# Optimization experiments

Hardware: AMD Instinct MI355X
Metric: run time of the kernel (lower is better)

Reference implementation:

```python
import jax, jax.numpy as jnp
import numpy as np

INPUT, HIDDEN, Z = 64, 256, 32


def setup_inputs() -> dict:
    key = jax.random.key(0)
    ks = jax.random.split(key, 16)
    B, T = 256, 1024
    s = lambda fan_in: 1.0 / np.sqrt(fan_in)
    u = lambda k, shape, b: jax.random.uniform(k, shape, jnp.float32, -b, b)
    return {
        "x": jax.random.normal(ks[0], (B, T, INPUT), jnp.float32),
        "eps": jax.random.normal(ks[1], (T, B, Z), jnp.float32),
        # encoder q(z|x,h): Linear(hidden+input -> z)
        "enc_mu_W": u(ks[2], (Z, HIDDEN + INPUT), s(HIDDEN + INPUT)),
        "enc_mu_b": u(ks[3], (Z,), s(HIDDEN + INPUT)),
        "enc_sigma_W": u(ks[4], (Z, HIDDEN + INPUT), s(HIDDEN + INPUT)),
        "enc_sigma_b": u(ks[5], (Z,), s(HIDDEN + INPUT)),
        # prior p(z|h): Linear(hidden -> z) (computed but unused, as in source)
        "prior_mu_W": u(ks[6], (Z, HIDDEN), s(HIDDEN)),
        "prior_mu_b": u(ks[7], (Z,), s(HIDDEN)),
        "prior_sigma_W": u(ks[8], (Z, HIDDEN), s(HIDDEN)),
        "prior_sigma_b": u(ks[9], (Z,), s(HIDDEN)),
        # GRU(input+z -> hidden), torch layout: [3H, in], gates order r,z,n
        "W_ih": u(ks[10], (3 * HIDDEN, INPUT + Z), s(HIDDEN)),
        "W_hh": u(ks[11], (3 * HIDDEN, HIDDEN), s(HIDDEN)),
        "b_ih": u(ks[12], (3 * HIDDEN,), s(HIDDEN)),
        "b_hh": u(ks[13], (3 * HIDDEN,), s(HIDDEN)),
    }


def _vrnn(x, eps, enc_mu_W, enc_mu_b, enc_sigma_W, enc_sigma_b,
          prior_mu_W, prior_mu_b, prior_sigma_W, prior_sigma_b,
          W_ih, W_hh, b_ih, b_hh):
    B = x.shape[0]
    x_t_first = jnp.transpose(x, (1, 0, 2))  # [T, B, input]
    h0 = jnp.zeros((B, HIDDEN), x.dtype)

    def step(h, inp):
        x_t, eps_t = inp
        # prior (dead code in source, kept for parity; DCE'd by XLA)
        _p_mu = h @ prior_mu_W.T + prior_mu_b
        _p_lv = h @ prior_sigma_W.T + prior_sigma_b
        enc_in = jnp.concatenate([x_t, h], axis=1)  # [B, input+hidden]
        z_mu = enc_in @ enc_mu_W.T + enc_mu_b
        z_logvar = enc_in @ enc_sigma_W.T + enc_sigma_b
        z_t = z_mu + eps_t * jnp.exp(0.5 * z_logvar)
        gru_in = jnp.concatenate([x_t, z_t], axis=1)  # [B, input+z]
        gi = gru_in @ W_ih.T + b_ih  # [B, 3H]
        gh = h @ W_hh.T + b_hh       # [B, 3H]
        i_r, i_z, i_n = jnp.split(gi, 3, axis=1)
        h_r, h_z, h_n = jnp.split(gh, 3, axis=1)
        r = jax.nn.sigmoid(i_r + h_r)
        u = jax.nn.sigmoid(i_z + h_z)
        n = jnp.tanh(i_n + r * h_n)
        h_new = (1.0 - u) * n + u * h
        return h_new, None

    h_last, _ = jax.lax.scan(step, h0, (x_t_first, eps))
    return h_last  # [B, hidden]


def reference(x, eps, enc_mu_W, enc_mu_b, enc_sigma_W, enc_sigma_b,
              prior_mu_W, prior_mu_b, prior_sigma_W, prior_sigma_b,
              W_ih, W_hh, b_ih, b_hh):
    return _vrnn(x, eps, enc_mu_W, enc_mu_b, enc_sigma_W, enc_sigma_b,
                 prior_mu_W, prior_mu_b, prior_sigma_W, prior_sigma_b,
                 W_ih, W_hh, b_ih, b_hh)
```

## Files before the change

kernel.cpp:

```cpp
#include <hip/hip_runtime.h>
#include <stdint.h>

#define NB 256
#define TSEQ 1024
#define TT_MAX 64

#define REG_P 12
#define LDS_P 24
#define STR_P 28
#define LDSTR 76

typedef _Float16 f16;
typedef _Float16 h2 __attribute__((ext_vector_type(2)));

static __device__ __forceinline__ uint32_t pkh2(float a, float b) {
  h2 v; v[0] = (f16)a; v[1] = (f16)b;
  return __builtin_bit_cast(uint32_t, v);
}

#if __has_builtin(__builtin_amdgcn_fdot2)
static __device__ __forceinline__ float dot2u(uint32_t w, uint32_t h, float c) {
  return __builtin_amdgcn_fdot2(__builtin_bit_cast(h2, w), __builtin_bit_cast(h2, h), c, false);
}
#else
static __device__ __forceinline__ float dot2u(uint32_t w, uint32_t h, float c) {
  h2 a = __builtin_bit_cast(h2, w), b = __builtin_bit_cast(h2, h);
  return c + (float)a[0] * (float)b[0] + (float)a[1] * (float)b[1];
}
#endif

#if __has_builtin(__builtin_amdgcn_rcpf)
#define RCPF(x) __builtin_amdgcn_rcpf(x)
#else
#define RCPF(x) (1.0f / (x))
#endif

static __device__ __forceinline__ float sigm(float x) {
  return RCPF(1.0f + exp2f(-1.44269504f * x));
}
static __device__ __forceinline__ float tanh_f(float x) {
  return 1.0f - 2.0f * RCPF(1.0f + exp2f(2.88539008f * x));
}

__global__ __launch_bounds__(512) void vrnn_pack(
    const float* __restrict__ W_hh, const float* __restrict__ W_ih,
    const float* __restrict__ emW, const float* __restrict__ esW,
    uint32_t* __restrict__ whr, uint32_t* __restrict__ whl,
    uint32_t* __restrict__ whs, uint32_t* __restrict__ whz,
    uint32_t* __restrict__ wep)
{
  const int t = threadIdx.x;
  const int r = t >> 1, q = t & 1;
  for (int rr = 0; rr < 3; ++rr) {
    const float* R = W_hh + (size_t)(r + rr * 256) * 256 + q * 128;
    for (int cj = 0; cj < 3; ++cj)
      for (int i = 0; i < 4; ++i) {
        int p = cj * 4 + i;
        whr[(((size_t)rr * 3 + cj) * 512 + t) * 4 + i] = pkh2(R[2 * p], R[2 * p + 1]);
      }
    for (int p = 0; p < LDS_P; ++p)
      whl[(size_t)t * LDSTR + rr * LDS_P + p] = pkh2(R[2 * (p + REG_P)], R[2 * (p + REG_P) + 1]);
    for (int j = 0; j < 7; ++j)
      for (int i = 0; i < 4; ++i) {
        int p = 36 + j * 4 + i;
        whs[(((size_t)rr * 7 + j) * 512 + t) * 4 + i] = pkh2(R[2 * p], R[2 * p + 1]);
      }
    const float* Z = W_ih + (size_t)(r + rr * 256) * 96 + 64 + q * 16;
    for (int cj = 0; cj < 2; ++cj)
      for (int i = 0; i < 4; ++i) {
        int p = cj * 4 + i;
        whz[(((size_t)rr * 2 + cj) * 512 + t) * 4 + i] = pkh2(Z[2 * p], Z[2 * p + 1]);
      }
  }
  {
    const int e = t & 63, s = t >> 6;
    const float* esrc = (e < 32) ? (emW + (size_t)e * 320 + 64)
                                 : (esW + (size_t)(e - 32) * 320 + 64);
    for (int p4 = 0; p4 < 4; ++p4)
      for (int i = 0; i < 4; ++i) {
        int pc = s * 16 + p4 * 4 + i;
        wep[((size_t)p4 * 512 + t) * 4 + i] = pkh2(esrc[2 * pc], esrc[2 * pc + 1]);
      }
  }
}

__global__ __launch_bounds__(256, 2) void vrnn_pre(
    const float* __restrict__ x, const float* __restrict__ W_ih,
    const float* __restrict__ b_ih, const float* __restrict__ b_hh,
    const float* __restrict__ emW, const float* __restrict__ emb,
    const float* __restrict__ esW, const float* __restrict__ esb,
    f16* __restrict__ gix, f16* __restrict__ zx,
    int chunk_t0, int TT, int nTT)
{
  const int tid = threadIdx.x;
  const int b  = blockIdx.x / nTT;
  const int tt = blockIdx.x % nTT;
  const int tloc0 = tt * TT;

  uint32_t wx[3][32];
  float bias[3];
  #pragma unroll
  for (int rr = 0; rr < 3; ++rr) {
    int j = tid + rr * 256;
    const float4* wr = (const float4*)(W_ih + (size_t)j * 96);
    #pragma unroll
    for (int p4 = 0; p4 < 16; ++p4) {
      float4 v = wr[p4];
      wx[rr][2 * p4]     = pkh2(v.x, v.y);
      wx[rr][2 * p4 + 1] = pkh2(v.z, v.w);
    }
    bias[rr] = b_ih[j] + (rr < 2 ? b_hh[j] : 0.0f);
  }
  uint32_t we[32]; float ebias = 0.0f;
  if (tid < 64) {
    const float* src = (tid < 32) ? (emW + (size_t)tid * 320)
                                  : (esW + (size_t)(tid - 32) * 320);
    #pragma unroll
    for (int p = 0; p < 32; ++p) we[p] = pkh2(src[2 * p], src[2 * p + 1]);
    ebias = (tid < 32) ? emb[tid] : esb[tid - 32];
  }

  __shared__ uint32_t xs[TT_MAX * 32];
  for (int idx = tid; idx < TT * 32; idx += 256) {
    int tl = idx >> 5, pk = idx & 31;
    size_t base = ((size_t)b * TSEQ + (chunk_t0 + tloc0 + tl)) * 64 + 2 * pk;
    xs[idx] = pkh2(x[base], x[base + 1]);
  }
  __syncthreads();

  for (int tl = 0; tl < TT; ++tl) {
    float a0 = bias[0], a1 = bias[1], a2 = bias[2];
    #pragma unroll
    for (int p = 0; p < 32; ++p) {
      uint32_t u = xs[tl * 32 + p];
      a0 = dot2u(wx[0][p], u, a0);
      a1 = dot2u(wx[1][p], u, a1);
      a2 = dot2u(wx[2][p], u, a2);
    }
    size_t ob = (size_t)(tloc0 + tl) * NB + b;
    f16* g = gix + ob * 768;
    g[tid] = (f16)a0; g[tid + 256] = (f16)a1; g[tid + 512] = (f16)a2;
    if (tid < 64) {
      float a3 = ebias;
      #pragma unroll
      for (int p = 0; p < 32; ++p) a3 = dot2u(we[p], xs[tl * 32 + p], a3);
      zx[ob * 64 + tid] = (f16)a3;
    }
  }
}

__global__ __launch_bounds__(512) void vrnn_rec(
    const f16* __restrict__ gix, const f16* __restrict__ zx,
    const float* __restrict__ eps,
    const uint32_t* __restrict__ whr, const uint32_t* __restrict__ whl_g,
    const uint32_t* __restrict__ whs, const uint32_t* __restrict__ whz,
    const uint32_t* __restrict__ wep_g,
    const float* __restrict__ b_hh,
    float* __restrict__ hws, float* __restrict__ out,
    int t0, int Tlen, int first, int last)
{
  const int t = threadIdx.x;
  const int b = blockIdx.x;
  const int r = t >> 1, q = t & 1;

  uint32_t wrg[3][REG_P];
  {
    const uint4* w4 = (const uint4*)whr;
    #pragma unroll
    for (int c = 0; c < 9; ++c) {
      uint4 v = w4[c * 512 + t];
      int rr = c / 3, p4 = c % 3;
      wrg[rr][4 * p4] = v.x; wrg[rr][4 * p4 + 1] = v.y;
      wrg[rr][4 * p4 + 2] = v.z; wrg[rr][4 * p4 + 3] = v.w;
    }
  }
  uint32_t wz[3][8];
  {
    const uint4* w4 = (const uint4*)whz;
    #pragma unroll
    for (int c = 0; c < 6; ++c) {
      uint4 v = w4[c * 512 + t];
      int rr = c / 2, p4 = c % 2;
      wz[rr][4 * p4] = v.x; wz[rr][4 * p4 + 1] = v.y;
      wz[rr][4 * p4 + 2] = v.z; wz[rr][4 * p4 + 3] = v.w;
    }
  }
  uint32_t we[16];
  {
    const uint4* w4 = (const uint4*)wep_g;
    #pragma unroll
    for (int c = 0; c < 4; ++c) {
      uint4 v = w4[c * 512 + t];
      we[4 * c] = v.x; we[4 * c + 1] = v.y; we[4 * c + 2] = v.z; we[4 * c + 3] = v.w;
    }
  }
  #pragma unroll
  for (int rr = 0; rr < 3; ++rr) {
    #pragma unroll
    for (int i = 0; i < REG_P; ++i) asm volatile("" : "+v"(wrg[rr][i]));
    #pragma unroll
    for (int i = 0; i < 8; ++i)    asm volatile("" : "+v"(wz[rr][i]));
  }
  #pragma unroll
  for (int i = 0; i < 16; ++i) asm volatile("" : "+v"(we[i]));
  const float bhn = b_hh[512 + r];

  __shared__ uint32_t lwh[512 * LDSTR];
  __shared__ __align__(16) f16 hf[2][264];
  __shared__ float encp[512];
  __shared__ uint32_t zu[16];

  {
    const uint4* src = (const uint4*)(whl_g + (size_t)t * LDSTR);
    uint4* dst = (uint4*)(lwh + (size_t)t * LDSTR);
    #pragma unroll
    for (int j = 0; j < LDSTR / 4; ++j) dst[j] = src[j];
  }

  const int hwидx = r + ((r >> 7) << 3);
  float hm = 0.0f;
  if (!q) {
    hm = first ? 0.0f : hws[b * 256 + r];
    hf[0][hwидx] = (f16)hm;
  }
  __syncthreads();

  float pf_g0 = 0.0f, pf_g1 = 0.0f, pf_g2 = 0.0f;
  if (!q) {
    const f16* gp0 = gix + (size_t)b * 768;
    pf_g0 = (float)gp0[r]; pf_g1 = (float)gp0[r + 256]; pf_g2 = (float)gp0[r + 512];
  }
  float pf_zm = 0.0f, pf_zl = 0.0f, pf_ep = 0.0f;
  if (t < 32) {
    const f16* zp = zx + (size_t)b * 64;
    pf_zm = (float)zp[t]; pf_zl = (float)zp[32 + t];
    pf_ep = eps[((size_t)t0 * NB + b) * 32 + t];
  }

  const int s = t >> 6;
  const int abase = 4 * s + (s >= 4 ? 1 : 0);
  const int bq = q ? 17 : 0;
  const uint32_t* myl = lwh + (size_t)t * LDSTR;
  const uint4* whs4 = (const uint4*)whs;

  uint4 sbuf[7];
  #pragma unroll
  for (int j = 0; j < 7; ++j) sbuf[j] = whs4[j * 512 + t];
  __builtin_amdgcn_sched_barrier(0);

  for (int tl = 0; tl < Tlen; ++tl) {
    const int cur = tl & 1, nxt = cur ^ 1;
    const uint4* hu4 = (const uint4*)&hf[cur][0];

    float ep_ = 0.0f;
    #pragma unroll
    for (int p4 = 0; p4 < 4; ++p4) {
      uint4 u4 = hu4[abase + p4];
      ep_ = dot2u(we[4 * p4],     u4.x, ep_);
      ep_ = dot2u(we[4 * p4 + 1], u4.y, ep_);
      ep_ = dot2u(we[4 * p4 + 2], u4.z, ep_);
      ep_ = dot2u(we[4 * p4 + 3], u4.w, ep_);
    }
    encp[t] = ep_;
    __syncthreads();

    if (t < 32) {
      float mu = pf_zm, lv = pf_zl;
      #pragma unroll
      for (int ss = 0; ss < 8; ++ss) {
        mu += encp[ss * 64 + t];
        lv += encp[ss * 64 + 32 + t];
      }
      float z = mu + pf_ep * exp2f(0.72134752f * lv);
      ((f16*)zu)[t] = (f16)z;
    }
    float g0 = 0.0f, g1 = 0.0f, g2 = 0.0f;
    #pragma unroll
    for (int g4 = 0; g4 < 3; ++g4) {
      uint4 u4 = hu4[bq + g4];
      g0 = dot2u(wrg[0][4 * g4],     u4.x, g0);
      g1 = dot2u(wrg[1][4 * g4],     u4.x, g1);
      g2 = dot2u(wrg[2][4 * g4],     u4.x, g2);
      g0 = dot2u(wrg[0][4 * g4 + 1], u4.y, g0);
      g1 = dot2u(wrg[1][4 * g4 + 1], u4.y, g1);
      g2 = dot2u(wrg[2][4 * g4 + 1], u4.y, g2);
      g0 = dot2u(wrg[0][4 * g4 + 2], u4.z, g0);
      g1 = dot2u(wrg[1][4 * g4 + 2], u4.z, g1);
      g2 = dot2u(wrg[2][4 * g4 + 2], u4.z, g2);
      g0 = dot2u(wrg[0][4 * g4 + 3], u4.w, g0);
      g1 = dot2u(wrg[1][4 * g4 + 3], u4.w, g1);
      g2 = dot2u(wrg[2][4 * g4 + 3], u4.w, g2);
    }
    {
      float a = 0.0f;
      #pragma unroll
      for (int j = 0; j < 7; ++j) {
        uint4 u4 = hu4[bq + 9 + j];
        a = dot2u(sbuf[j].x, u4.x, a);
        a = dot2u(sbuf[j].y, u4.y, a);
        a = dot2u(sbuf[j].z, u4.z, a);
        a = dot2u(sbuf[j].w, u4.w, a);
      }
      g0 += a;
    }
    #pragma unroll
    for (int j = 0; j < 7; ++j) sbuf[j] = whs4[(7 + j) * 512 + t];
    __builtin_amdgcn_sched_barrier(0);
    #pragma unroll
    for (int g4 = 0; g4 < 3; ++g4) {
      uint4 u4 = hu4[bq + 3 + g4];
      uint4 w0 = *(const uint4*)(myl + 0 * LDS_P + 4 * g4);
      uint4 w1 = *(const uint4*)(myl + 1 * LDS_P + 4 * g4);
      uint4 w2 = *(const uint4*)(myl + 2 * LDS_P + 4 * g4);
      g0 = dot2u(w0.x, u4.x, g0); g1 = dot2u(w1.x, u4.x, g1); g2 = dot2u(w2.x, u4.x, g2);
      g0 = dot2u(w0.y, u4.y, g0); g1 = dot2u(w1.y, u4.y, g1); g2 = dot2u(w2.y, u4.y, g2);
      g0 = dot2u(w0.z, u4.z, g0); g1 = dot2u(w1.z, u4.z, g1); g2 = dot2u(w2.z, u4.z, g2);
      g0 = dot2u(w0.w, u4.w, g0); g1 = dot2u(w1.w, u4.w, g1); g2 = dot2u(w2.w, u4.w, g2);
    }
    {
      float a = 0.0f;
      #pragma unroll
      for (int j = 0; j < 7; ++j) {
        uint4 u4 = hu4[bq + 9 + j];
        a = dot2u(sbuf[j].x, u4.x, a);
        a = dot2u(sbuf[j].y, u4.y, a);
        a = dot2u(sbuf[j].z, u4.z, a);
        a = dot2u(sbuf[j].w, u4.w, a);
      }
      g1 += a;
    }
    #pragma unroll
    for (int j = 0; j < 7; ++j) sbuf[j] = whs4[(14 + j) * 512 + t];
    __builtin_amdgcn_sched_barrier(0);
    #pragma unroll
    for (int g4 = 3; g4 < 6; ++g4) {
      uint4 u4 = hu4[bq + 3 + g4];
      uint4 w0 = *(const uint4*)(myl + 0 * LDS_P + 4 * g4);
      uint4 w1 = *(const uint4*)(myl + 1 * LDS_P + 4 * g4);
      uint4 w2 = *(const uint4*)(myl + 2 * LDS_P + 4 * g4);
      g0 = dot2u(w0.x, u4.x, g0); g1 = dot2u(w1.x, u4.x, g1); g2 = dot2u(w2.x, u4.x, g2);
      g0 = dot2u(w0.y, u4.y, g0); g1 = dot2u(w1.y, u4.y, g1); g2 = dot2u(w2.y, u4.y, g2);
      g0 = dot2u(w0.z, u4.z, g0); g1 = dot2u(w1.z, u4.z, g1); g2 = dot2u(w2.z, u4.z, g2);
      g0 = dot2u(w0.w, u4.w, g0); g1 = dot2u(w1.w, u4.w, g1); g2 = dot2u(w2.w, u4.w, g2);
    }
    {
      float a = 0.0f;
      #pragma unroll
      for (int j = 0; j < 7; ++j) {
        uint4 u4 = hu4[bq + 9 + j];
        a = dot2u(sbuf[j].x, u4.x, a);
        a = dot2u(sbuf[j].y, u4.y, a);
        a = dot2u(sbuf[j].z, u4.z, a);
        a = dot2u(sbuf[j].w, u4.w, a);
      }
      g2 += a;
    }
    __syncthreads();

    float q0 = 0.0f, q1 = 0.0f, q2 = 0.0f;
    #pragma unroll
    for (int p = 0; p < 8; ++p) {
      uint32_t u = zu[q * 8 + p];
      q0 = dot2u(wz[0][p], u, q0);
      q1 = dot2u(wz[1][p], u, q1);
      q2 = dot2u(wz[2][p], u, q2);
    }
    g0 += __shfl_xor(g0, 1); g1 += __shfl_xor(g1, 1); g2 += __shfl_xor(g2, 1);
    q0 += __shfl_xor(q0, 1); q1 += __shfl_xor(q1, 1); q2 += __shfl_xor(q2, 1);
    if (!q) {
      float rg = sigm(pf_g0 + g0 + q0);
      float uu = sigm(pf_g1 + g1 + q1);
      float n  = tanh_f(pf_g2 + q2 + rg * (g2 + bhn));
      hm = (1.0f - uu) * n + uu * hm;
      hf[nxt][hwидx] = (f16)hm;
    }

    #pragma unroll
    for (int j = 0; j < 7; ++j) sbuf[j] = whs4[j * 512 + t];
    __builtin_amdgcn_sched_barrier(0);

    int tn = (tl + 1 < Tlen) ? tl + 1 : tl;
    if (!q) {
      const f16* gp = gix + ((size_t)tn * NB + b) * 768;
      pf_g0 = (float)gp[r]; pf_g1 = (float)gp[r + 256]; pf_g2 = (float)gp[r + 512];
    }
    if (t < 32) {
      const f16* zp = zx + ((size_t)tn * NB + b) * 64;
      pf_zm = (float)zp[t]; pf_zl = (float)zp[32 + t];
      pf_ep = eps[((size_t)(t0 + tn) * NB + b) * 32 + t];
    }
    __syncthreads();
  }

  if (!q) {
    if (last) out[b * 256 + r] = hm;
    else      hws[b * 256 + r] = hm;
  }
}

extern "C" void kernel_launch(void* const* d_in, const int* in_sizes, int n_in,
                              void* d_out, int out_size, void* d_ws, size_t ws_size,
                              hipStream_t stream) {
  const float* x    = (const float*)d_in[0];
  const float* eps  = (const float*)d_in[1];
  const float* emW  = (const float*)d_in[2];
  const float* emb  = (const float*)d_in[3];
  const float* esW  = (const float*)d_in[4];
  const float* esb  = (const float*)d_in[5];
  const float* W_ih = (const float*)d_in[10];
  const float* W_hh = (const float*)d_in[11];
  const float* b_ih = (const float*)d_in[12];
  const float* b_hh = (const float*)d_in[13];
  float* out = (float*)d_out;

  const size_t o_whr = 262144;
  const size_t o_whl = o_whr + 73728;
  const size_t o_whs = o_whl + 155648;
  const size_t o_whz = o_whs + 172032;
  const size_t o_wep = o_whz + 49152;
  const size_t o_gix = o_wep + 32768;
  int Tc = TSEQ;
  while (Tc > 8 && o_gix + (size_t)Tc * NB * (768 + 64) * 2 > ws_size) Tc >>= 1;

  float*    hws   = (float*)d_ws;
  uint32_t* whr   = (uint32_t*)((char*)d_ws + o_whr);
  uint32_t* whl_g = (uint32_t*)((char*)d_ws + o_whl);
  uint32_t* whs   = (uint32_t*)((char*)d_ws + o_whs);
  uint32_t* whz   = (uint32_t*)((char*)d_ws + o_whz);
  uint32_t* wep   = (uint32_t*)((char*)d_ws + o_wep);
  f16*      gix   = (f16*)((char*)d_ws + o_gix);
  f16*      zx    = gix + (size_t)Tc * NB * 768;

  vrnn_pack<<<dim3(1), dim3(512), 0, stream>>>(W_hh, W_ih, emW, esW,
                                               whr, whl_g, whs, whz, wep);

  int nch = TSEQ / Tc;
  int TT  = Tc < 64 ? Tc : 64;
  int nTT = Tc / TT;

  for (int c = 0; c < nch; ++c) {
    vrnn_pre<<<dim3(NB * nTT), dim3(256), 0, stream>>>(
        x, W_ih, b_ih, b_hh, emW, emb, esW, esb, gix, zx, c * Tc, TT, nTT);
    vrnn_rec<<<dim3(NB), dim3(512), 0, stream>>>(
        gix, zx, eps, whr, whl_g, whs, whz, wep, b_hh, hws, out,
        c * Tc, Tc, c == 0 ? 1 : 0, c == nch - 1 ? 1 : 0);
  }
}
```

Measured before the change: 2.623 ms.

## Move more W_hh columns into registers and rebalance streamed weight chunks

The per-thread W_hh split changes: register-resident pairs go from 12 to 16 per gate, and the per-step streamed chunks drop from 7 uint4 (one gate each) to 6 uint4 covering all three gates across two h quads. The streamed phases now accumulate directly into g0/g1/g2, interleaving all gates, instead of using a separate accumulator per gate. This cuts global/L2 weight traffic per timestep and adds independent dot chains. The cost is higher VGPR pressure, which could cause spills or lower occupancy.

Measured after the change: 2.534 ms (median of 2 runs). 1.04x faster.

```diff
diff --git a/kernel.cpp b/kernel.cpp
--- a/kernel.cpp
+++ b/kernel.cpp
@@ -5,9 +5,8 @@
 #define TSEQ 1024
 #define TT_MAX 64
 
-#define REG_P 12
+#define REG_P 16
 #define LDS_P 24
-#define STR_P 28
 #define LDSTR 76
 
 typedef _Float16 f16;
@@ -53,18 +52,19 @@
   const int r = t >> 1, q = t & 1;
   for (int rr = 0; rr < 3; ++rr) {
     const float* R = W_hh + (size_t)(r + rr * 256) * 256 + q * 128;
-    for (int cj = 0; cj < 3; ++cj)
+    for (int cj = 0; cj < 4; ++cj)
       for (int i = 0; i < 4; ++i) {
         int p = cj * 4 + i;
-        whr[(((size_t)rr * 3 + cj) * 512 + t) * 4 + i] = pkh2(R[2 * p], R[2 * p + 1]);
+        whr[(((size_t)rr * 4 + cj) * 512 + t) * 4 + i] = pkh2(R[2 * p], R[2 * p + 1]);
       }
     for (int p = 0; p < LDS_P; ++p)
       whl[(size_t)t * LDSTR + rr * LDS_P + p] = pkh2(R[2 * (p + REG_P)], R[2 * (p + REG_P) + 1]);
-    for (int j = 0; j < 7; ++j)
-      for (int i = 0; i < 4; ++i) {
-        int p = 36 + j * 4 + i;
-        whs[(((size_t)rr * 7 + j) * 512 + t) * 4 + i] = pkh2(R[2 * p], R[2 * p + 1]);
-      }
+    for (int m = 0; m < 3; ++m)
+      for (int k = 0; k < 2; ++k)
+        for (int i = 0; i < 4; ++i) {
+          int p = (10 + 2 * m + k) * 4 + i;
+          whs[(((size_t)m * 6 + rr * 2 + k) * 512 + t) * 4 + i] = pkh2(R[2 * p], R[2 * p + 1]);
+        }
     const float* Z = W_ih + (size_t)(r + rr * 256) * 96 + 64 + q * 16;
     for (int cj = 0; cj < 2; ++cj)
       for (int i = 0; i < 4; ++i) {
@@ -167,9 +167,9 @@
   {
     const uint4* w4 = (const uint4*)whr;
     #pragma unroll
-    for (int c = 0; c < 9; ++c) {
+    for (int c = 0; c < 12; ++c) {
       uint4 v = w4[c * 512 + t];
-      int rr = c / 3, p4 = c % 3;
+      int rr = c >> 2, p4 = c & 3;
       wrg[rr][4 * p4] = v.x; wrg[rr][4 * p4 + 1] = v.y;
       wrg[rr][4 * p4 + 2] = v.z; wrg[rr][4 * p4 + 3] = v.w;
     }
@@ -180,7 +180,7 @@
     #pragma unroll
     for (int c = 0; c < 6; ++c) {
       uint4 v = w4[c * 512 + t];
-      int rr = c / 2, p4 = c % 2;
+      int rr = c >> 1, p4 = c & 1;
       wz[rr][4 * p4] = v.x; wz[rr][4 * p4 + 1] = v.y;
       wz[rr][4 * p4 + 2] = v.z; wz[rr][4 * p4 + 3] = v.w;
     }
@@ -217,11 +217,11 @@
     for (int j = 0; j < LDSTR / 4; ++j) dst[j] = src[j];
   }
 
-  const int hwидx = r + ((r >> 7) << 3);
+  const int hwidx = r + ((r >> 7) << 3);
   float hm = 0.0f;
   if (!q) {
     hm = first ? 0.0f : hws[b * 256 + r];
-    hf[0][hwидx] = (f16)hm;
+    hf[0][hwidx] = (f16)hm;
   }
   __syncthreads();
 
@@ -243,9 +243,9 @@
   const uint32_t* myl = lwh + (size_t)t * LDSTR;
   const uint4* whs4 = (const uint4*)whs;
 
-  uint4 sbuf[7];
+  uint4 sbuf[6];
   #pragma unroll
-  for (int j = 0; j < 7; ++j) sbuf[j] = whs4[j * 512 + t];
+  for (int j = 0; j < 6; ++j) sbuf[j] = whs4[j * 512 + t];
   __builtin_amdgcn_sched_barrier(0);
 
   for (int tl = 0; tl < Tlen; ++tl) {
@@ -276,7 +276,7 @@
     }
     float g0 = 0.0f, g1 = 0.0f, g2 = 0.0f;
     #pragma unroll
-    for (int g4 = 0; g4 < 3; ++g4) {
+    for (int g4 = 0; g4 < 4; ++g4) {
       uint4 u4 = hu4[bq + g4];
       g0 = dot2u(wrg[0][4 * g4],     u4.x, g0);
       g1 = dot2u(wrg[1][4 * g4],     u4.x, g1);
@@ -292,23 +292,26 @@
       g2 = dot2u(wrg[2][4 * g4 + 3], u4.w, g2);
     }
     {
-      float a = 0.0f;
-      #pragma unroll
-      for (int j = 0; j < 7; ++j) {
-        uint4 u4 = hu4[bq + 9 + j];
-        a = dot2u(sbuf[j].x, u4.x, a);
-        a = dot2u(sbuf[j].y, u4.y, a);
-        a = dot2u(sbuf[j].z, u4.z, a);
-        a = dot2u(sbuf[j].w, u4.w, a);
-      }
-      g0 += a;
-    }
-    #pragma unroll
-    for (int j = 0; j < 7; ++j) sbuf[j] = whs4[(7 + j) * 512 + t];
+      uint4 hq0 = hu4[bq + 10], hq1 = hu4[bq + 11];
+      g0 = dot2u(sbuf[0].x, hq0.x, g0); g0 = dot2u(sbuf[0].y, hq0.y, g0);
+      g0 = dot2u(sbuf[0].z, hq0.z, g0); g0 = dot2u(sbuf[0].w, hq0.w, g0);
+      g1 = dot2u(sbuf[2].x, hq0.x, g1); g1 = dot2u(sbuf[2].y, hq0.y, g1);
+      g1 = dot2u(sbuf[2].z, hq0.z, g1); g1 = dot2u(sbuf[2].w, hq0.w, g1);
+      g2 = dot2u(sbuf[4].x, hq0.x, g2); g2 = dot2u(sbuf[4].y, hq0.y, g2);
+      g2 = dot2u(sbuf[4].z, hq0.z, g2); g2 = dot2u(sbuf[4].w, hq0.w, g2);
+      g0 = dot2u(sbuf[1].x, hq1.x, g0); g0 = dot2u(sbuf[1].y, hq1.y, g0);
+      g0 = dot2u(sbuf[1].z, hq1.z, g0); g0 = dot2u(sbuf[1].w, hq1.w, g0);
+      g1 = dot2u(sbuf[3].x, hq1.x, g1); g1 = dot2u(sbuf[3].y, hq1.y, g1);
+      g1 = dot2u(sbuf[3].z, hq1.z, g1); g1 = dot2u(sbuf[3].w, hq1.w, g1);
+      g2 = dot2u(sbuf[5].x, hq1.x, g2); g2 = dot2u(sbuf[5].y, hq1.y, g2);
+      g2 = dot2u(sbuf[5].z, hq1.z, g2); g2 = dot2u(sbuf[5].w, hq1.w, g2);
+    }
+    #pragma unroll
+    for (int j = 0; j < 6; ++j) sbuf[j] = whs4[(6 + j) * 512 + t];
     __builtin_amdgcn_sched_barrier(0);
     #pragma unroll
     for (int g4 = 0; g4 < 3; ++g4) {
-      uint4 u4 = hu4[bq + 3 + g4];
+      uint4 u4 = hu4[bq + 4 + g4];
       uint4 w0 = *(const uint4*)(myl + 0 * LDS_P + 4 * g4);
       uint4 w1 = *(const uint4*)(myl + 1 * LDS_P + 4 * g4);
       uint4 w2 = *(const uint4*)(myl + 2 * LDS_P + 4 * g4);
@@ -318,23 +321,26 @@
       g0 = dot2u(w0.w, u4.w, g0); g1 = dot2u(w1.w, u4.w, g1); g2 = dot2u(w2.w, u4.w, g2);
     }
     {
-      float a = 0.0f;
-      #pragma unroll
-      for (int j = 0; j < 7; ++j) {
-        uint4 u4 = hu4[bq + 9 + j];
-        a = dot2u(sbuf[j].x, u4.x, a);
-        a = dot2u(sbuf[j].y, u4.y, a);
-        a = dot2u(sbuf[j].z, u4.z, a);
-        a = dot2u(sbuf[j].w, u4.w, a);
-      }
-      g1 += a;
-    }
-    #pragma unroll
-    for (int j = 0; j < 7; ++j) sbuf[j] = whs4[(14 + j) * 512 + t];
+      uint4 hq0 = hu4[bq + 12], hq1 = hu4[bq + 13];
+      g0 = dot2u(sbuf[0].x, hq0.x, g0); g0 = dot2u(sbuf[0].y, hq0.y, g0);
+      g0 = dot2u(sbuf[0].z, hq0.z, g0); g0 = dot2u(sbuf[0].w, hq0.w, g0);
+      g1 = dot2u(sbuf[2].x, hq0.x, g1); g1 = dot2u(sbuf[2].y, hq0.y, g1);
+      g1 = dot2u(sbuf[2].z, hq0.z, g1); g1 = dot2u(sbuf[2].w, hq0.w, g1);
+      g2 = dot2u(sbuf[4].x, hq0.x, g2); g2 = dot2u(sbuf[4].y, hq0.y, g2);
+      g2 = dot2u(sbuf[4].z, hq0.z, g2); g2 = dot2u(sbuf[4].w, hq0.w, g2);
+      g0 = dot2u(sbuf[1].x, hq1.x, g0); g0 = dot2u(sbuf[1].y, hq1.y, g0);
+      g0 = dot2u(sbuf[1].z, hq1.z, g0); g0 = dot2u(sbuf[1].w, hq1.w, g0);
+      g1 = dot2u(sbuf[3].x, hq1.x, g1); g1 = dot2u(sbuf[3].y, hq1.y, g1);
+      g1 = dot2u(sbuf[3].z, hq1.z, g1); g1 = dot2u(sbuf[3].w, hq1.w, g1);
+      g2 = dot2u(sbuf[5].x, hq1.x, g2); g2 = dot2u(sbuf[5].y, hq1.y, g2);
+      g2 = dot2u(sbuf[5].z, hq1.z, g2); g2 = dot2u(sbuf[5].w, hq1.w, g2);
+    }
+    #pragma unroll
+    for (int j = 0; j < 6; ++j) sbuf[j] = whs4[(12 + j) * 512 + t];
     __builtin_amdgcn_sched_barrier(0);
     #pragma unroll
     for (int g4 = 3; g4 < 6; ++g4) {
-      uint4 u4 = hu4[bq + 3 + g4];
+      uint4 u4 = hu4[bq + 4 + g4];
       uint4 w0 = *(const uint4*)(myl + 0 * LDS_P + 4 * g4);
       uint4 w1 = *(const uint4*)(myl + 1 * LDS_P + 4 * g4);
       uint4 w2 = *(const uint4*)(myl + 2 * LDS_P + 4 * g4);
@@ -344,16 +350,19 @@
       g0 = dot2u(w0.w, u4.w, g0); g1 = dot2u(w1.w, u4.w, g1); g2 = dot2u(w2.w, u4.w, g2);
     }
     {
-      float a = 0.0f;
-      #pragma unroll
-      for (int j = 0; j < 7; ++j) {
-        uint4 u4 = hu4[bq + 9 + j];
-        a = dot2u(sbuf[j].x, u4.x, a);
-        a = dot2u(sbuf[j].y, u4.y, a);
-        a = dot2u(sbuf[j].z, u4.z, a);
-        a = dot2u(sbuf[j].w, u4.w, a);
-      }
-      g2 += a;
+      uint4 hq0 = hu4[bq + 14], hq1 = hu4[bq + 15];
+      g0 = dot2u(sbuf[0].x, hq0.x, g0); g0 = dot2u(sbuf[0].y, hq0.y, g0);
+      g0 = dot2u(sbuf[0].z, hq0.z, g0); g0 = dot2u(sbuf[0].w, hq0.w, g0);
+      g1 = dot2u(sbuf[2].x, hq0.x, g1); g1 = dot2u(sbuf[2].y, hq0.y, g1);
+      g1 = dot2u(sbuf[2].z, hq0.z, g1); g1 = dot2u(sbuf[2].w, hq0.w, g1);
+      g2 = dot2u(sbuf[4].x, hq0.x, g2); g2 = dot2u(sbuf[4].y, hq0.y, g2);
+      g2 = dot2u(sbuf[4].z, hq0.z, g2); g2 = dot2u(sbuf[4].w, hq0.w, g2);
+      g0 = dot2u(sbuf[1].x, hq1.x, g0); g0 = dot2u(sbuf[1].y, hq1.y, g0);
+      g0 = dot2u(sbuf[1].z, hq1.z, g0); g0 = dot2u(sbuf[1].w, hq1.w, g0);
+      g1 = dot2u(sbuf[3].x, hq1.x, g1); g1 = dot2u(sbuf[3].y, hq1.y, g1);
+      g1 = dot2u(sbuf[3].z, hq1.z, g1); g1 = dot2u(sbuf[3].w, hq1.w, g1);
+      g2 = dot2u(sbuf[5].x, hq1.x, g2); g2 = dot2u(sbuf[5].y, hq1.y, g2);
+      g2 = dot2u(sbuf[5].z, hq1.z, g2); g2 = dot2u(sbuf[5].w, hq1.w, g2);
     }
     __syncthreads();
 
@@ -372,11 +381,11 @@
       float uu = sigm(pf_g1 + g1 + q1);
       float n  = tanh_f(pf_g2 + q2 + rg * (g2 + bhn));
       hm = (1.0f - uu) * n + uu * hm;
-      hf[nxt][hwидx] = (f16)hm;
-    }
-
-    #pragma unroll
-    for (int j = 0; j < 7; ++j) sbuf[j] = whs4[j * 512 + t];
+      hf[nxt][hwidx] = (f16)hm;
+    }
+
+    #pragma unroll
+    for (int j = 0; j < 6; ++j) sbuf[j] = whs4[j * 512 + t];
     __builtin_amdgcn_sched_barrier(0);
 
     int tn = (tl + 1 < Tlen) ? tl + 1 : tl;
@@ -414,9 +423,9 @@
   float* out = (float*)d_out;
 
   const size_t o_whr = 262144;
-  const size_t o_whl = o_whr + 73728;
+  const size_t o_whl = o_whr + 98304;
   const size_t o_whs = o_whl + 155648;
-  const size_t o_whz = o_whs + 172032;
+  const size_t o_whz = o_whs + 147456;
   const size_t o_wep = o_whz + 49152;
   const size_t o_gix = o_wep + 32768;
   int Tc = TSEQ;
```

## Reorder streamed W_hh chunks into a triple-buffered rolling prefetch pipeline

Applied to the files above, without the earlier changes.

Repacks the global-streamed part of W_hh so each 16-byte chunk index holds all three gates. The recurrent step now consumes and reissues loads in a rotating three-slot buffer, interleaved with the LDS-resident dot products, replacing three separate 7-deep sequential batches. The aim is a steadier load pipeline that hides global-memory latency behind the LDS work, without the stalls at each batch boundary. Register use changes from 7 to 9 uint4 buffers, which could raise register pressure.

New measurement: 2.576 ms. About the same (-1.8%).

```diff
diff --git a/kernel.cpp b/kernel.cpp
--- a/kernel.cpp
+++ b/kernel.cpp
@@ -7,7 +7,6 @@
 
 #define REG_P 12
 #define LDS_P 24
-#define STR_P 28
 #define LDSTR 76
 
 typedef _Float16 f16;
@@ -60,10 +59,10 @@
       }
     for (int p = 0; p < LDS_P; ++p)
       whl[(size_t)t * LDSTR + rr * LDS_P + p] = pkh2(R[2 * (p + REG_P)], R[2 * (p + REG_P) + 1]);
-    for (int j = 0; j < 7; ++j)
+    for (int c = 0; c < 7; ++c)
       for (int i = 0; i < 4; ++i) {
-        int p = 36 + j * 4 + i;
-        whs[(((size_t)rr * 7 + j) * 512 + t) * 4 + i] = pkh2(R[2 * p], R[2 * p + 1]);
+        int p = (9 + c) * 4 + i;
+        whs[(((size_t)c * 3 + rr) * 512 + t) * 4 + i] = pkh2(R[2 * p], R[2 * p + 1]);
       }
     const float* Z = W_ih + (size_t)(r + rr * 256) * 96 + 64 + q * 16;
     for (int cj = 0; cj < 2; ++cj)
@@ -148,6 +147,31 @@
     }
   }
 }
+
+#define CONS(B0, B1, B2, HQI) { \
+  uint4 hq = hu4[HQI]; \
+  g0 = dot2u(B0.x, hq.x, g0); g0 = dot2u(B0.y, hq.y, g0); \
+  g0 = dot2u(B0.z, hq.z, g0); g0 = dot2u(B0.w, hq.w, g0); \
+  g1 = dot2u(B1.x, hq.x, g1); g1 = dot2u(B1.y, hq.y, g1); \
+  g1 = dot2u(B1.z, hq.z, g1); g1 = dot2u(B1.w, hq.w, g1); \
+  g2 = dot2u(B2.x, hq.x, g2); g2 = dot2u(B2.y, hq.y, g2); \
+  g2 = dot2u(B2.z, hq.z, g2); g2 = dot2u(B2.w, hq.w, g2); }
+
+#define ISS(B0, B1, B2, C) { \
+  B0 = whs4[((C) * 3 + 0) * 512 + t]; \
+  B1 = whs4[((C) * 3 + 1) * 512 + t]; \
+  B2 = whs4[((C) * 3 + 2) * 512 + t]; \
+  __builtin_amdgcn_sched_barrier(0); }
+
+#define LQ(G) { \
+  uint4 u4 = hu4[bq + 3 + (G)]; \
+  uint4 w0 = *(const uint4*)(myl + 0 * LDS_P + 4 * (G)); \
+  uint4 w1 = *(const uint4*)(myl + 1 * LDS_P + 4 * (G)); \
+  uint4 w2 = *(const uint4*)(myl + 2 * LDS_P + 4 * (G)); \
+  g0 = dot2u(w0.x, u4.x, g0); g1 = dot2u(w1.x, u4.x, g1); g2 = dot2u(w2.x, u4.x, g2); \
+  g0 = dot2u(w0.y, u4.y, g0); g1 = dot2u(w1.y, u4.y, g1); g2 = dot2u(w2.y, u4.y, g2); \
+  g0 = dot2u(w0.z, u4.z, g0); g1 = dot2u(w1.z, u4.z, g1); g2 = dot2u(w2.z, u4.z, g2); \
+  g0 = dot2u(w0.w, u4.w, g0); g1 = dot2u(w1.w, u4.w, g1); g2 = dot2u(w2.w, u4.w, g2); }
 
 __global__ __launch_bounds__(512) void vrnn_rec(
     const f16* __restrict__ gix, const f16* __restrict__ zx,
@@ -180,7 +204,7 @@
     #pragma unroll
     for (int c = 0; c < 6; ++c) {
       uint4 v = w4[c * 512 + t];
-      int rr = c / 2, p4 = c % 2;
+      int rr = c >> 1, p4 = c & 1;
       wz[rr][4 * p4] = v.x; wz[rr][4 * p4 + 1] = v.y;
       wz[rr][4 * p4 + 2] = v.z; wz[rr][4 * p4 + 3] = v.w;
     }
@@ -217,11 +241,11 @@
     for (int j = 0; j < LDSTR / 4; ++j) dst[j] = src[j];
   }
 
-  const int hwидx = r + ((r >> 7) << 3);
+  const int hwidx = r + ((r >> 7) << 3);
   float hm = 0.0f;
   if (!q) {
     hm = first ? 0.0f : hws[b * 256 + r];
-    hf[0][hwидx] = (f16)hm;
+    hf[0][hwidx] = (f16)hm;
   }
   __syncthreads();
 
@@ -243,10 +267,10 @@
   const uint32_t* myl = lwh + (size_t)t * LDSTR;
   const uint4* whs4 = (const uint4*)whs;
 
-  uint4 sbuf[7];
-  #pragma unroll
-  for (int j = 0; j < 7; ++j) sbuf[j] = whs4[j * 512 + t];
-  __builtin_amdgcn_sched_barrier(0);
+  uint4 sa0, sa1, sa2, sb0, sb1, sb2, sc0, sc1, sc2;
+  ISS(sa0, sa1, sa2, 0)
+  ISS(sb0, sb1, sb2, 1)
+  ISS(sc0, sc1, sc2, 2)
 
   for (int tl = 0; tl < Tlen; ++tl) {
     const int cur = tl & 1, nxt = cur ^ 1;
@@ -291,70 +315,19 @@
       g1 = dot2u(wrg[1][4 * g4 + 3], u4.w, g1);
       g2 = dot2u(wrg[2][4 * g4 + 3], u4.w, g2);
     }
-    {
-      float a = 0.0f;
-      #pragma unroll
-      for (int j = 0; j < 7; ++j) {
-        uint4 u4 = hu4[bq + 9 + j];
-        a = dot2u(sbuf[j].x, u4.x, a);
-        a = dot2u(sbuf[j].y, u4.y, a);
-        a = dot2u(sbuf[j].z, u4.z, a);
-        a = dot2u(sbuf[j].w, u4.w, a);
-      }
-      g0 += a;
-    }
-    #pragma unroll
-    for (int j = 0; j < 7; ++j) sbuf[j] = whs4[(7 + j) * 512 + t];
-    __builtin_amdgcn_sched_barrier(0);
-    #pragma unroll
-    for (int g4 = 0; g4 < 3; ++g4) {
-      uint4 u4 = hu4[bq + 3 + g4];
-      uint4 w0 = *(const uint4*)(myl + 0 * LDS_P + 4 * g4);
-      uint4 w1 = *(const uint4*)(myl + 1 * LDS_P + 4 * g4);
-      uint4 w2 = *(const uint4*)(myl + 2 * LDS_P + 4 * g4);
-      g0 = dot2u(w0.x, u4.x, g0); g1 = dot2u(w1.x, u4.x, g1); g2 = dot2u(w2.x, u4.x, g2);
-      g0 = dot2u(w0.y, u4.y, g0); g1 = dot2u(w1.y, u4.y, g1); g2 = dot2u(w2.y, u4.y, g2);
-      g0 = dot2u(w0.z, u4.z, g0); g1 = dot2u(w1.z, u4.z, g1); g2 = dot2u(w2.z, u4.z, g2);
-      g0 = dot2u(w0.w, u4.w, g0); g1 = dot2u(w1.w, u4.w, g1); g2 = dot2u(w2.w, u4.w, g2);
-    }
-    {
-      float a = 0.0f;
-      #pragma unroll
-      for (int j = 0; j < 7; ++j) {
-        uint4 u4 = hu4[bq + 9 + j];
-        a = dot2u(sbuf[j].x, u4.x, a);
-        a = dot2u(sbuf[j].y, u4.y, a);
-        a = dot2u(sbuf[j].z, u4.z, a);
-        a = dot2u(sbuf[j].w, u4.w, a);
-      }
-      g1 += a;
-    }
-    #pragma unroll
-    for (int j = 0; j < 7; ++j) sbuf[j] = whs4[(14 + j) * 512 + t];
-    __builtin_amdgcn_sched_barrier(0);
-    #pragma unroll
-    for (int g4 = 3; g4 < 6; ++g4) {
-      uint4 u4 = hu4[bq + 3 + g4];
-      uint4 w0 = *(const uint4*)(myl + 0 * LDS_P + 4 * g4);
-      uint4 w1 = *(const uint4*)(myl + 1 * LDS_P + 4 * g4);
-      uint4 w2 = *(const uint4*)(myl + 2 * LDS_P + 4 * g4);
-      g0 = dot2u(w0.x, u4.x, g0); g1 = dot2u(w1.x, u4.x, g1); g2 = dot2u(w2.x, u4.x, g2);
-      g0 = dot2u(w0.y, u4.y, g0); g1 = dot2u(w1.y, u4.y, g1); g2 = dot2u(w2.y, u4.y, g2);
-      g0 = dot2u(w0.z, u4.z, g0); g1 = dot2u(w1.z, u4.z, g1); g2 = dot2u(w2.z, u4.z, g2);
-      g0 = dot2u(w0.w, u4.w, g0); g1 = dot2u(w1.w, u4.w, g1); g2 = dot2u(w2.w, u4.w, g2);
-    }
-    {
-      float a = 0.0f;
-      #pragma unroll
-      for (int j = 0; j < 7; ++j) {
-        uint4 u4 = hu4[bq + 9 + j];
-        a = dot2u(sbuf[j].x, u4.x, a);
-        a = dot2u(sbuf[j].y, u4.y, a);
-        a = dot2u(sbuf[j].z, u4.z, a);
-        a = dot2u(sbuf[j].w, u4.w, a);
-      }
-      g2 += a;
-    }
+    CONS(sa0, sa1, sa2, bq + 9)   ISS(sa0, sa1, sa2, 3)
+    LQ(0)
+    CONS(sb0, sb1, sb2, bq + 10)  ISS(sb0, sb1, sb2, 4)
+    LQ(1)
+    CONS(sc0, sc1, sc2, bq + 11)  ISS(sc0, sc1, sc2, 5)
+    LQ(2)
+    CONS(sa0, sa1, sa2, bq + 12)  ISS(sa0, sa1, sa2, 6)
+    LQ(3)
+    CONS(sb0, sb1, sb2, bq + 13)
+    LQ(4)
+    CONS(sc0, sc1, sc2, bq + 14)
+    LQ(5)
+    CONS(sa0, sa1, sa2, bq + 15)
     __syncthreads();
 
     float q0 = 0.0f, q1 = 0.0f, q2 = 0.0f;
@@ -372,12 +345,12 @@
       float uu = sigm(pf_g1 + g1 + q1);
       float n  = tanh_f(pf_g2 + q2 + rg * (g2 + bhn));
       hm = (1.0f - uu) * n + uu * hm;
-      hf[nxt][hwидx] = (f16)hm;
-    }
-
-    #pragma unroll
-    for (int j = 0; j < 7; ++j) sbuf[j] = whs4[j * 512 + t];
-    __builtin_amdgcn_sched_barrier(0);
+      hf[nxt][hwidx] = (f16)hm;
+    }
+
+    ISS(sa0, sa1, sa2, 0)
+    ISS(sb0, sb1, sb2, 1)
+    ISS(sc0, sc1, sc2, 2)
 
     int tn = (tl + 1 < Tlen) ? tl + 1 : tl;
     if (!q) {
```
